# Kernel tuning notes

Hardware: AMD Instinct MI355X
Metric: run time of the kernel (lower is better)

The kernel has to match this reference:

```python
import jax, jax.numpy as jnp
import numpy as np

HEADS = 8
DIM_HEAD = 64
SCALE = DIM_HEAD ** -0.5


def setup_inputs() -> dict:
    key = jax.random.key(0)
    ks = jax.random.split(key, 7)
    B, N, Dq = 2, 4096, 512
    M, Dc = 4096, 768
    inner = HEADS * DIM_HEAD  # 512
    x = jax.random.normal(ks[0], (B, N, Dq), dtype=jnp.float32)
    context = jax.random.normal(ks[1], (B, M, Dc), dtype=jnp.float32)
    # weights stored [in, out] (torch Linear weight transposed)
    Wq = jax.random.normal(ks[2], (Dq, inner), dtype=jnp.float32) * (Dq ** -0.5)
    Wk = jax.random.normal(ks[3], (Dc, inner), dtype=jnp.float32) * (Dc ** -0.5)
    Wv = jax.random.normal(ks[4], (Dc, inner), dtype=jnp.float32) * (Dc ** -0.5)
    Wo = jax.random.normal(ks[5], (inner, Dq), dtype=jnp.float32) * (inner ** -0.5)
    bo = jax.random.normal(ks[6], (Dq,), dtype=jnp.float32) * 0.01
    return {"x": x, "context": context, "Wq": Wq, "Wk": Wk, "Wv": Wv, "Wo": Wo, "bo": bo}


def reference(x, context, Wq, Wk, Wv, Wo, bo):
    B, N, _ = x.shape
    M = context.shape[1]
    h, d = HEADS, DIM_HEAD
    q = (x @ Wq).reshape(B, N, h, d)                      # b n h d
    k = ((context @ Wk) * SCALE).reshape(B, M, h, d)      # scale applied to k, as in source
    v = (context @ Wv).reshape(B, M, h, d)
    scores = jnp.einsum('bnhd,bmhd->bhnm', q, k)          # full QK^T
    attn = jax.nn.softmax(scores, axis=-1)
    out = jnp.einsum('bhnm,bmhd->bnhd', attn, v).reshape(B, N, h * d)
    return out @ Wo + bo  # dropout p=0.0 -> identity
```

## Files before the change

kernel.cpp:

```cpp
#include <hip/hip_runtime.h>

typedef unsigned short u16;
typedef __attribute__((ext_vector_type(4))) unsigned short u16x4;
typedef __attribute__((ext_vector_type(8))) unsigned short u16x8;
typedef __attribute__((ext_vector_type(8))) short s16x8;
typedef __attribute__((ext_vector_type(4))) float f32x4;
typedef __attribute__((ext_vector_type(16))) float f32x16;
typedef __attribute__((ext_vector_type(4))) unsigned int u32x4;

#define LOG2E 1.4426950408889634f

__device__ __forceinline__ u16 f2bf(float f) {
    return __builtin_bit_cast(unsigned short, static_cast<__bf16>(f));
}

__device__ __forceinline__ float bf2f(u16 v) {
    return __builtin_bit_cast(float, (unsigned)v << 16);
}

__device__ __forceinline__ float fexp2(float x) {
#if __has_builtin(__builtin_amdgcn_exp2f)
    return __builtin_amdgcn_exp2f(x);
#else
    return exp2f(x);
#endif
}

__device__ __forceinline__ s16x8 ld_frag(const u16* p) {
    return __builtin_bit_cast(s16x8, *reinterpret_cast<const u16x8*>(p));
}

__device__ __forceinline__ f32x4 mfma16(s16x8 a, s16x8 b, f32x4 c) {
    return __builtin_amdgcn_mfma_f32_16x16x32_bf16(a, b, c, 0, 0, 0);
}

__device__ __forceinline__ f32x16 mfma32(s16x8 a, s16x8 b, f32x16 c) {
    return __builtin_amdgcn_mfma_f32_32x32x16_bf16(a, b, c, 0, 0, 0);
}

__device__ __forceinline__ unsigned cvt_pk_bf16(float lo, float hi2) {
    unsigned r;
    asm("v_cvt_pk_bf16_f32 %0, %1, %2" : "=v"(r) : "v"(lo), "v"(hi2));
    return r;
}

__device__ __forceinline__ void plane32_swap(unsigned& x, unsigned& y) {
#if __has_builtin(__builtin_amdgcn_permlane32_swap)
    auto r = __builtin_amdgcn_permlane32_swap(x, y, false, false);
    x = r[0];
    y = r[1];
#else
    asm("v_permlane32_swap_b32 %0, %1" : "+v"(x), "+v"(y));
#endif
}

__device__ __forceinline__ void async16(const u16* g, u16* lds) {
    __builtin_amdgcn_global_load_lds(
        (__attribute__((address_space(1))) void*)const_cast<u16*>(g),
        (__attribute__((address_space(3))) void*)lds, 16, 0, 0);
}

__global__ __launch_bounds__(256) void cvt_fused_kernel(const float* __restrict__ x,
                                                        const float* __restrict__ ctx,
                                                        u16* __restrict__ xb,
                                                        u16* __restrict__ cb) {
    int i = blockIdx.x * 256 + threadIdx.x;
    const float* in;
    u16* out;
    int idx;
    if (i < 524288) {
        in = x; out = xb; idx = i;
    } else {
        in = ctx; out = cb; idx = i - 524288;
    }
    const f32x4* p = (const f32x4*)in + ((size_t)idx << 1);
    f32x4 a = p[0], c = p[1];
    u16x8 v;
    v[0] = f2bf(a[0]); v[1] = f2bf(a[1]); v[2] = f2bf(a[2]); v[3] = f2bf(a[3]);
    v[4] = f2bf(c[0]); v[5] = f2bf(c[1]); v[6] = f2bf(c[2]); v[7] = f2bf(c[3]);
    *((u16x8*)out + idx) = v;
}

__global__ __launch_bounds__(256) void wtrans4_kernel(
    const float* __restrict__ Wq, const float* __restrict__ Wk, const float* __restrict__ Wv,
    const float* __restrict__ Wo, u16* __restrict__ Wqt, u16* __restrict__ Wkt,
    u16* __restrict__ Wvt, u16* __restrict__ Wot) {
    __shared__ float t[32][33];
    const float* W;
    u16* Wt;
    int Kd;
    float scale;
    switch (blockIdx.z) {
        case 0: W = Wq; Wt = Wqt; Kd = 512; scale = 1.0f; break;
        case 1: W = Wk; Wt = Wkt; Kd = 768; scale = 0.125f * LOG2E; break;
        case 2: W = Wv; Wt = Wvt; Kd = 768; scale = 1.0f; break;
        default: W = Wo; Wt = Wot; Kd = 512; scale = 1.0f; break;
    }
    const int k0 = blockIdx.x << 5, n0 = blockIdx.y << 5;
    if (k0 >= Kd) return;
    const int tx = threadIdx.x, ty = threadIdx.y;
#pragma unroll
    for (int i = 0; i < 32; i += 8)
        t[ty + i][tx] = W[(size_t)(k0 + ty + i) * 512 + n0 + tx] * scale;
    __syncthreads();
#pragma unroll
    for (int i = 0; i < 32; i += 8)
        Wt[(size_t)(n0 + ty + i) * Kd + k0 + tx] = f2bf(t[tx][ty + i]);
}

template <int MODE>
__device__ __forceinline__ void gemm_body(u16* __restrict__ Ab, u16* __restrict__ Bb,
                                          const u16* __restrict__ A, const u16* __restrict__ Bt,
                                          void* __restrict__ Cv, const float* __restrict__ bias,
                                          int K) {
    const int tid = threadIdx.x;
    const int w = tid >> 6, l = tid & 63;
    const int lg = l >> 4, lq = l & 15;
    const int wm = w >> 1, wn = w & 1;
    const int bm = blockIdx.y, bn = blockIdx.x;
    const int KT = K >> 6;

    f32x4 acc[4][4];
#pragma unroll
    for (int i = 0; i < 4; i++)
#pragma unroll
        for (int j = 0; j < 4; j++) acc[i][j] = (f32x4){0.f, 0.f, 0.f, 0.f};

    const u16* Ag0 = A + (size_t)bm * 128 * K;
    const u16* Bg0 = Bt + (size_t)bn * 128 * K;
    const int srow = l >> 3, scol = (l & 7) << 3;

    auto stage = [&](int kt, int buf) {
#pragma unroll
        for (int i = 0; i < 4; i++) {
            const int c = (w << 2) + i;
            const int row = (c << 3) + srow;
            async16(Ag0 + (size_t)row * K + kt * 64 + scol, Ab + (buf << 13) + (c << 9));
            async16(Bg0 + (size_t)row * K + kt * 64 + scol, Bb + (buf << 13) + (c << 9));
        }
    };

    stage(0, 0);
    for (int kt = 0; kt < KT; ++kt) {
        __syncthreads();
        if (kt + 1 < KT) stage(kt + 1, (kt + 1) & 1);
        const u16* As = Ab + ((kt & 1) << 13);
        const u16* Bs = Bb + ((kt & 1) << 13);
#pragma unroll
        for (int s = 0; s < 2; s++) {
            s16x8 af[4], bfr[4];
#pragma unroll
            for (int mt = 0; mt < 4; mt++)
                af[mt] = ld_frag(As + ((wm << 6) + (mt << 4) + lq) * 64 + (s << 5) + (lg << 3));
#pragma unroll
            for (int nt = 0; nt < 4; nt++)
                bfr[nt] = ld_frag(Bs + ((wn << 6) + (nt << 4) + lq) * 64 + (s << 5) + (lg << 3));
#pragma unroll
            for (int mt = 0; mt < 4; mt++)
#pragma unroll
                for (int nt = 0; nt < 4; nt++)
                    acc[mt][nt] = mfma16(af[mt], bfr[nt], acc[mt][nt]);
        }
    }
    const int row0 = bm * 128 + (wm << 6);
    const int col0 = bn * 128 + (wn << 6);
    if constexpr (MODE == 0) {
        u16* C = (u16*)Cv;
#pragma unroll
        for (int mt = 0; mt < 4; mt++)
#pragma unroll
            for (int nt = 0; nt < 4; nt++)
#pragma unroll
                for (int r = 0; r < 4; r++)
                    C[(size_t)(row0 + (mt << 4) + (lg << 2) + r) * 512 + col0 + (nt << 4) + lq] =
                        f2bf(acc[mt][nt][r]);
    } else if constexpr (MODE == 3) {
        float* C = (float*)Cv;
        float bv[4];
#pragma unroll
        for (int nt = 0; nt < 4; nt++) bv[nt] = bias[col0 + (nt << 4) + lq];
#pragma unroll
        for (int mt = 0; mt < 4; mt++)
#pragma unroll
            for (int nt = 0; nt < 4; nt++)
#pragma unroll
                for (int r = 0; r < 4; r++)
                    C[(size_t)(row0 + (mt << 4) + (lg << 2) + r) * 512 + col0 + (nt << 4) + lq] =
                        acc[mt][nt][r] + bv[nt];
    } else {
        u16* C = (u16*)Cv;
#pragma unroll
        for (int mt = 0; mt < 4; mt++)
#pragma unroll
            for (int nt = 0; nt < 4; nt++)
#pragma unroll
                for (int r = 0; r < 4; r++) {
                    const int m = row0 + (mt << 4) + (lg << 2) + r;
                    const int feat = col0 + (nt << 4) + lq;
                    const int bh = ((m >> 12) << 3) + (feat >> 6);
                    const int d = feat & 63;
                    const int kv = m & 4095;
                    const int T = kv >> 5, kvl = kv & 31;
                    size_t off;
                    if constexpr (MODE == 1) {
                        const int lane = kvl + (((d >> 3) & 1) << 5);
                        off = ((size_t)(((bh << 7) + T) << 2) + (d >> 4)) * 512 + (lane << 3) +
                              (d & 7);
                    } else {
                        const int lane = (d & 31) + (((kvl >> 3) & 1) << 5);
                        const int fi = ((kvl >> 4) << 1) + (d >> 5);
                        off = ((size_t)(((bh << 7) + T) << 2) + fi) * 512 + (lane << 3) +
                              (kvl & 7);
                    }
                    C[off] = f2bf(acc[mt][nt][r]);
                }
    }
}

__global__ __launch_bounds__(256, 2) void proj_gemm_kernel(
    const u16* __restrict__ xb, const u16* __restrict__ cb, const u16* __restrict__ Wqt,
    const u16* __restrict__ Wkt, const u16* __restrict__ Wvt, u16* __restrict__ Qb,
    u16* __restrict__ Kp, u16* __restrict__ Vp) {
    __shared__ u16 Ab[2][8192];
    __shared__ u16 Bb[2][8192];
    const int z = blockIdx.z;
    if (z == 0)
        gemm_body<0>(&Ab[0][0], &Bb[0][0], xb, Wqt, Qb, nullptr, 512);
    else if (z == 1)
        gemm_body<1>(&Ab[0][0], &Bb[0][0], cb, Wkt, Kp, nullptr, 768);
    else
        gemm_body<2>(&Ab[0][0], &Bb[0][0], cb, Wvt, Vp, nullptr, 768);
}

__global__ __launch_bounds__(256, 2) void out_gemm_kernel(const u16* __restrict__ Ob,
                                                          const u16* __restrict__ Wot,
                                                          float* __restrict__ out,
                                                          const float* __restrict__ bias) {
    __shared__ u16 Ab[2][8192];
    __shared__ u16 Bb[2][8192];
    gemm_body<3>(&Ab[0][0], &Bb[0][0], Ob, Wot, out, bias, 512);
}

__global__ __launch_bounds__(128, 3) void attn_kernel(const u16* __restrict__ Qb,
                                                      const u16* __restrict__ Kp,
                                                      const u16* __restrict__ Vp,
                                                      u16* __restrict__ Opart,
                                                      float* __restrict__ Lpart) {
    const int tid = threadIdx.x;
    const int w = tid >> 6, l = tid & 63;
    const int lq = l & 31, hi = l >> 5;
    const int bid = blockIdx.x;
    const int swz = ((bid & 7) << 9) + (bid >> 3);
    const int wid = (swz << 1) + w;
    const int kvseg = wid & 3, qt = (wid >> 2) & 127, bh = wid >> 9;
    const int b = bh >> 3, h = bh & 7;

    const u16* Qp = Qb + (size_t)(b * 4096 + (qt << 5) + lq) * 512 + (h << 6) + (hi << 3);
    s16x8 qf[4];
#pragma unroll
    for (int s = 0; s < 4; s++) qf[s] = ld_frag(Qp + (s << 4));

    const u16* Kg = Kp + ((size_t)(bh << 7) + (kvseg << 5)) * 2048 + (l << 3);
    const u16* Vg = Vp + ((size_t)(bh << 7) + (kvseg << 5)) * 2048 + (l << 3);

    f32x16 oacc0 = {}, oacc1 = {}, ls = {};
    const f32x16 zc = {};

    s16x8 onesb;
#pragma unroll
    for (int j = 0; j < 8; j++) onesb[j] = 0x3F80;

    s16x8 kA[4], vA[4], kB[4], vB[4];
#pragma unroll
    for (int f = 0; f < 4; f++) {
        kA[f] = ld_frag(Kg + (f << 9));
        vA[f] = ld_frag(Vg + (f << 9));
    }

    const u16* kptr = Kg + 2048;
    const u16* vptr = Vg + 2048;

    auto body = [&](s16x8 (&kf)[4], s16x8 (&vf)[4], s16x8 (&kn)[4], s16x8 (&vn)[4],
                    const bool pref) {
        if (pref) {
#pragma unroll
            for (int f = 0; f < 4; f++) {
                kn[f] = ld_frag(kptr + (f << 9));
                vn[f] = ld_frag(vptr + (f << 9));
            }
            kptr += 2048;
            vptr += 2048;
        }
        __builtin_amdgcn_s_setprio(1);
        f32x16 sacc = mfma32(kf[0], qf[0], zc);
#pragma unroll
        for (int s = 1; s < 4; s++) sacc = mfma32(kf[s], qf[s], sacc);
        __builtin_amdgcn_s_setprio(0);
#pragma unroll
        for (int r = 0; r < 16; r++) sacc[r] = fexp2(sacc[r]);
        s16x8 aw[2];
#pragma unroll
        for (int sp = 0; sp < 2; sp++) {
            const int base2 = sp << 3;
            unsigned X1 = cvt_pk_bf16(sacc[base2 + 0], sacc[base2 + 1]);
            unsigned Y1 = cvt_pk_bf16(sacc[base2 + 4], sacc[base2 + 5]);
            unsigned X2 = cvt_pk_bf16(sacc[base2 + 2], sacc[base2 + 3]);
            unsigned Y2 = cvt_pk_bf16(sacc[base2 + 6], sacc[base2 + 7]);
            plane32_swap(X1, Y1);
            plane32_swap(X2, Y2);
            u32x4 wv;
            wv[0] = X1; wv[1] = X2; wv[2] = Y1; wv[3] = Y2;
            aw[sp] = __builtin_bit_cast(s16x8, wv);
        }
        __builtin_amdgcn_s_setprio(1);
#pragma unroll
        for (int sp = 0; sp < 2; sp++) {
            ls = mfma32(aw[sp], onesb, ls);
            oacc0 = mfma32(aw[sp], vf[(sp << 1) + 0], oacc0);
            oacc1 = mfma32(aw[sp], vf[(sp << 1) + 1], oacc1);
        }
        __builtin_amdgcn_s_setprio(0);
    };

    for (int i = 0; i < 15; ++i) {
        body(kA, vA, kB, vB, true);
        body(kB, vB, kA, vA, true);
    }
    body(kA, vA, kB, vB, true);
    body(kB, vB, kA, vA, false);

    u16* Ow = Opart + ((size_t)wid << 11);
#pragma unroll
    for (int r = 0; r < 16; r++) Ow[(r << 6) + l] = f2bf(oacc0[r]);
#pragma unroll
    for (int r = 0; r < 16; r++) Ow[((16 + r) << 6) + l] = f2bf(oacc1[r]);
    if (lq == 0) {
#pragma unroll
        for (int r = 0; r < 16; r++)
            Lpart[(wid << 5) + (r & 3) + ((r >> 2) << 3) + (hi << 2)] = ls[r];
    }
}

__global__ __launch_bounds__(256) void merge_kernel(const u16* __restrict__ Op,
                                                    const float* __restrict__ Lp,
                                                    u16* __restrict__ Ob) {
    const int g = blockIdx.x * 256 + threadIdx.x;
    const int slot = g >> 9;
    const int idx4 = (g & 511) << 2;
    const int dtr = idx4 >> 6;
    const int r = dtr & 15, dt = dtr >> 4;
    const int lane0 = idx4 & 63;
    const int q = (r & 3) + ((r >> 2) << 3) + ((lane0 >> 5) << 2);
    float lsum = 0.f;
#pragma unroll
    for (int p = 0; p < 4; p++) lsum += Lp[(slot << 7) + (p << 5) + q];
    const float ri = 1.f / lsum;
    float acc[4] = {0.f, 0.f, 0.f, 0.f};
#pragma unroll
    for (int p = 0; p < 4; p++) {
        const u16x4 a = *(const u16x4*)(Op + ((size_t)slot << 13) + (p << 11) + idx4);
#pragma unroll
        for (int j = 0; j < 4; j++) acc[j] += bf2f(a[j]);
    }
    u16x4 o;
#pragma unroll
    for (int j = 0; j < 4; j++) o[j] = f2bf(acc[j] * ri);
    const int bh = slot >> 7, qt = slot & 127;
    const int row = ((bh >> 3) << 12) + (qt << 5) + q;
    const int d = (lane0 & 31) + (dt << 5);
    *(u16x4*)(Ob + (size_t)row * 512 + ((bh & 7) << 6) + d) = o;
}

extern "C" void kernel_launch(void* const* d_in, const int* in_sizes, int n_in, void* d_out,
                              int out_size, void* d_ws, size_t ws_size, hipStream_t stream) {
    const float* x = (const float*)d_in[0];
    const float* ctx = (const float*)d_in[1];
    const float* Wq = (const float*)d_in[2];
    const float* Wk = (const float*)d_in[3];
    const float* Wv = (const float*)d_in[4];
    const float* Wo = (const float*)d_in[5];
    const float* bo = (const float*)d_in[6];
    float* out = (float*)d_out;

    char* ws = (char*)d_ws;
    u16* xb  = (u16*)(ws);
    u16* cb  = (u16*)(ws + 8388608);
    u16* Opart   = (u16*)(ws);
    float* Lpart = (float*)(ws + 33554432);
    u16* Qb  = (u16*)(ws + 34603008);
    u16* Ob  = (u16*)(ws + 34603008);
    u16* Kp  = (u16*)(ws + 42991616);
    u16* Vp  = (u16*)(ws + 51380224);
    u16* Wqt = (u16*)(ws + 59768832);
    u16* Wkt = (u16*)(ws + 60293120);
    u16* Wvt = (u16*)(ws + 61079552);
    u16* Wot = (u16*)(ws + 61865984);

    cvt_fused_kernel<<<dim3(5120), dim3(256), 0, stream>>>(x, ctx, xb, cb);
    wtrans4_kernel<<<dim3(24, 16, 4), dim3(32, 8), 0, stream>>>(Wq, Wk, Wv, Wo, Wqt, Wkt, Wvt,
                                                                Wot);
    proj_gemm_kernel<<<dim3(4, 64, 3), dim3(256), 0, stream>>>(xb, cb, Wqt, Wkt, Wvt, Qb, Kp, Vp);
    attn_kernel<<<dim3(4096), dim3(128), 0, stream>>>(Qb, Kp, Vp, Opart, Lpart);
    merge_kernel<<<dim3(4096), dim3(256), 0, stream>>>(Opart, Lpart, Ob);
    out_gemm_kernel<<<dim3(4, 64), dim3(256), 0, stream>>>(Ob, Wot, out, bo);
}
```

Baseline: 174.2 us.

## Share K/V tiles across four query-tile waves via async LDS double buffering

```diff
diff --git a/kernel.cpp b/kernel.cpp
--- a/kernel.cpp
+++ b/kernel.cpp
@@ -241,18 +241,21 @@
     gemm_body<3>(&Ab[0][0], &Bb[0][0], Ob, Wot, out, bias, 512);
 }
 
-__global__ __launch_bounds__(128, 3) void attn_kernel(const u16* __restrict__ Qb,
+__global__ __launch_bounds__(256, 3) void attn_kernel(const u16* __restrict__ Qb,
                                                       const u16* __restrict__ Kp,
                                                       const u16* __restrict__ Vp,
                                                       u16* __restrict__ Opart,
                                                       float* __restrict__ Lpart) {
+    __shared__ u16 Kl[2][2048];
+    __shared__ u16 Vl[2][2048];
     const int tid = threadIdx.x;
     const int w = tid >> 6, l = tid & 63;
     const int lq = l & 31, hi = l >> 5;
     const int bid = blockIdx.x;
-    const int swz = ((bid & 7) << 9) + (bid >> 3);
-    const int wid = (swz << 1) + w;
-    const int kvseg = wid & 3, qt = (wid >> 2) & 127, bh = wid >> 9;
+    const int swz = ((bid & 7) << 8) + (bid >> 3);
+    const int bh = swz >> 7, qtg = (swz >> 2) & 31, kvseg = swz & 3;
+    const int qt = (qtg << 2) + w;
+    const int wid = (((bh << 7) + qt) << 2) + kvseg;
     const int b = bh >> 3, h = bh & 7;
 
     const u16* Qp = Qb + (size_t)(b * 4096 + (qt << 5) + lq) * 512 + (h << 6) + (hi << 3);
@@ -260,44 +263,47 @@
 #pragma unroll
     for (int s = 0; s < 4; s++) qf[s] = ld_frag(Qp + (s << 4));
 
-    const u16* Kg = Kp + ((size_t)(bh << 7) + (kvseg << 5)) * 2048 + (l << 3);
-    const u16* Vg = Vp + ((size_t)(bh << 7) + (kvseg << 5)) * 2048 + (l << 3);
-
-    f32x16 oacc0 = {}, oacc1 = {}, ls = {};
-    const f32x16 zc = {};
-
-    s16x8 onesb;
-#pragma unroll
-    for (int j = 0; j < 8; j++) onesb[j] = 0x3F80;
-
-    s16x8 kA[4], vA[4], kB[4], vB[4];
-#pragma unroll
-    for (int f = 0; f < 4; f++) {
-        kA[f] = ld_frag(Kg + (f << 9));
-        vA[f] = ld_frag(Vg + (f << 9));
-    }
-
-    const u16* kptr = Kg + 2048;
-    const u16* vptr = Vg + 2048;
-
-    auto body = [&](s16x8 (&kf)[4], s16x8 (&vf)[4], s16x8 (&kn)[4], s16x8 (&vn)[4],
-                    const bool pref) {
-        if (pref) {
-#pragma unroll
-            for (int f = 0; f < 4; f++) {
-                kn[f] = ld_frag(kptr + (f << 9));
-                vn[f] = ld_frag(vptr + (f << 9));
-            }
-            kptr += 2048;
-            vptr += 2048;
-        }
+    const u16* Kg = Kp + ((size_t)(bh << 7) + (kvseg << 5)) * 2048;
+    const u16* Vg = Vp + ((size_t)(bh << 7) + (kvseg << 5)) * 2048;
+    const int gsrc = (w << 9) + (l << 3);
+    const int ldst = w << 9;
+    const int roff = l << 3;
+
+    f32x16 oacc0 = {}, oacc1 = {};
+    float rs = 0.f;
+
+    async16(Kg + gsrc, &Kl[0][ldst]);
+    async16(Vg + gsrc, &Vl[0][ldst]);
+
+    for (int t = 0; t < 32; ++t) {
+        const int buf = t & 1;
+        __syncthreads();
+        if (t + 1 < 32) {
+            async16(Kg + (size_t)(t + 1) * 2048 + gsrc, &Kl[buf ^ 1][ldst]);
+            async16(Vg + (size_t)(t + 1) * 2048 + gsrc, &Vl[buf ^ 1][ldst]);
+        }
+        const u16* Kb_ = Kl[buf];
+        const u16* Vb_ = Vl[buf];
+
+        s16x8 kf[4];
+#pragma unroll
+        for (int s = 0; s < 4; s++) kf[s] = ld_frag(Kb_ + (s << 9) + roff);
+        f32x16 sacc = {};
         __builtin_amdgcn_s_setprio(1);
-        f32x16 sacc = mfma32(kf[0], qf[0], zc);
-#pragma unroll
-        for (int s = 1; s < 4; s++) sacc = mfma32(kf[s], qf[s], sacc);
+#pragma unroll
+        for (int s = 0; s < 4; s++) sacc = mfma32(kf[s], qf[s], sacc);
         __builtin_amdgcn_s_setprio(0);
+
 #pragma unroll
         for (int r = 0; r < 16; r++) sacc[r] = fexp2(sacc[r]);
+        {
+            float t0 = (sacc[0] + sacc[1]) + (sacc[2] + sacc[3]);
+            float t1 = (sacc[4] + sacc[5]) + (sacc[6] + sacc[7]);
+            float t2 = (sacc[8] + sacc[9]) + (sacc[10] + sacc[11]);
+            float t3 = (sacc[12] + sacc[13]) + (sacc[14] + sacc[15]);
+            rs += (t0 + t1) + (t2 + t3);
+        }
+
         s16x8 aw[2];
 #pragma unroll
         for (int sp = 0; sp < 2; sp++) {
@@ -312,33 +318,26 @@
             wv[0] = X1; wv[1] = X2; wv[2] = Y1; wv[3] = Y2;
             aw[sp] = __builtin_bit_cast(s16x8, wv);
         }
+
+        s16x8 vf[4];
+#pragma unroll
+        for (int f = 0; f < 4; f++) vf[f] = ld_frag(Vb_ + (f << 9) + roff);
         __builtin_amdgcn_s_setprio(1);
 #pragma unroll
         for (int sp = 0; sp < 2; sp++) {
-            ls = mfma32(aw[sp], onesb, ls);
             oacc0 = mfma32(aw[sp], vf[(sp << 1) + 0], oacc0);
             oacc1 = mfma32(aw[sp], vf[(sp << 1) + 1], oacc1);
         }
         __builtin_amdgcn_s_setprio(0);
-    };
-
-    for (int i = 0; i < 15; ++i) {
-        body(kA, vA, kB, vB, true);
-        body(kB, vB, kA, vA, true);
-    }
-    body(kA, vA, kB, vB, true);
-    body(kB, vB, kA, vA, false);
+    }
 
     u16* Ow = Opart + ((size_t)wid << 11);
 #pragma unroll
     for (int r = 0; r < 16; r++) Ow[(r << 6) + l] = f2bf(oacc0[r]);
 #pragma unroll
     for (int r = 0; r < 16; r++) Ow[((16 + r) << 6) + l] = f2bf(oacc1[r]);
-    if (lq == 0) {
-#pragma unroll
-        for (int r = 0; r < 16; r++)
-            Lpart[(wid << 5) + (r & 3) + ((r >> 2) << 3) + (hi << 2)] = ls[r];
-    }
+    rs += __shfl_xor(rs, 32);
+    if (l < 32) Lpart[(wid << 5) + l] = rs;
 }
 
 __global__ __launch_bounds__(256) void merge_kernel(const u16* __restrict__ Op,
@@ -400,7 +399,7 @@
     wtrans4_kernel<<<dim3(24, 16, 4), dim3(32, 8), 0, stream>>>(Wq, Wk, Wv, Wo, Wqt, Wkt, Wvt,
                                                                 Wot);
     proj_gemm_kernel<<<dim3(4, 64, 3), dim3(256), 0, stream>>>(xb, cb, Wqt, Wkt, Wvt, Qb, Kp, Vp);
-    attn_kernel<<<dim3(4096), dim3(128), 0, stream>>>(Qb, Kp, Vp, Opart, Lpart);
+    attn_kernel<<<dim3(2048), dim3(256), 0, stream>>>(Qb, Kp, Vp, Opart, Lpart);
     merge_kernel<<<dim3(4096), dim3(256), 0, stream>>>(Opart, Lpart, Ob);
     out_gemm_kernel<<<dim3(4, 64), dim3(256), 0, stream>>>(Ob, Wot, out, bo);
 }
```

After: 156.2 us. -10.4%, faster.
